# Kernel optimization log

Hardware: AMD Instinct MI355X
Metric: run time of the kernel (lower is better)

The kernel has to match this reference:

```python
import jax, jax.numpy as jnp
import numpy as np

N_NODES = 50000
N_PAIRS = 1_600_000
D_IN = 128
D_OUT = 128


def setup_inputs() -> dict:
    key = jax.random.key(0)
    k1, k2, k3, k4, k5, k6 = jax.random.split(key, 6)
    features = jax.random.normal(k1, (N_NODES, D_IN), dtype=jnp.float32)
    pair_w = jax.random.uniform(k2, (N_PAIRS,), dtype=jnp.float32)  # cosine weights per pair
    # Xavier-uniform init for the projection weight, zeros for bias (as in torch module)
    limit = float(np.sqrt(6.0 / (D_IN + D_OUT)))
    weight = jax.random.uniform(k3, (D_IN, D_OUT), dtype=jnp.float32, minval=-limit, maxval=limit)
    bias = jnp.zeros((D_OUT,), dtype=jnp.float32)
    pair_i = jax.random.randint(k4, (N_PAIRS,), 0, N_NODES)
    pair_j = jax.random.randint(k5, (N_PAIRS,), 0, N_NODES)
    node_idx = jnp.sort(jax.random.randint(k6, (N_PAIRS,), 0, N_NODES))  # center node per pair
    return {"features": features, "pair_w": pair_w, "weight": weight, "bias": bias,
            "pair_i": pair_i, "pair_j": pair_j, "node_idx": node_idx}


def reference(features, pair_w, weight, bias, pair_i, pair_j, node_idx):
    # Per pair: (features[i] + features[j]) * cos_weight  -> [n_pairs, d_in]
    msgs = (features[pair_i] + features[pair_j]) * pair_w[:, None]
    # Accumulate into the center node of each pair -> [n_nodes, d_in]
    agg = jax.ops.segment_sum(msgs, node_idx, num_segments=N_NODES)
    # Final linear projection
    return agg @ weight + bias
```

## Files before the change

### kernel.cpp

```cpp
#include <hip/hip_runtime.h>

#define D 128

__device__ __forceinline__ float bf_lo(unsigned u) { return __uint_as_float(u << 16); }
__device__ __forceinline__ float bf_hi(unsigned u) { return __uint_as_float(u & 0xffff0000u); }
__device__ __forceinline__ unsigned pack_bf16(float a, float b) {
    unsigned ua = __float_as_uint(a), ub = __float_as_uint(b);
    ua = (ua + 0x7fffu + ((ua >> 16) & 1u)) >> 16;
    ub = (ub + 0x7fffu + ((ub >> 16) & 1u)) >> 16;
    return ua | (ub << 16);
}

__global__ __launch_bounds__(256) void cvt_bf16_kernel(const float* __restrict__ F,
                                                       unsigned* __restrict__ Fb, int n4) {
    int t = blockIdx.x * 256 + threadIdx.x;
    if (t >= n4) return;
    float4 v = reinterpret_cast<const float4*>(F)[t];
    uint2 o = {pack_bf16(v.x, v.y), pack_bf16(v.z, v.w)};
    reinterpret_cast<uint2*>(Fb)[t] = o;
}

__global__ __launch_bounds__(256) void wcvt_kernel(const float* __restrict__ W,
                                                   unsigned* __restrict__ Wb) {
    int t = blockIdx.x * 256 + threadIdx.x;
    if (t >= D * D / 2) return;
    Wb[t] = pack_bf16(W[2 * t], W[2 * t + 1]);
}

__global__ void prepack_kernel(const int* __restrict__ pi, const int* __restrict__ pj,
                               const float* __restrict__ pw, const int* __restrict__ nidx,
                               uint2* __restrict__ rec, int* __restrict__ offs,
                               int n_pairs, int n_nodes) {
    int p = blockIdx.x * 256 + threadIdx.x;
    if (p >= n_pairs) return;
    rec[p] = make_uint2((unsigned)pi[p] | ((unsigned)pj[p] << 16), __float_as_uint(pw[p]));
    int cur  = nidx[p];
    int prev = p ? nidx[p - 1] : -1;
    for (int n = prev + 1; n <= cur; ++n) offs[n] = p;
    if (p == n_pairs - 1)
        for (int n = cur + 1; n <= n_nodes; ++n) offs[n] = n_pairs;
}

__global__ __launch_bounds__(256) void aggregate_kernel(
    const unsigned* __restrict__ Fb, const uint2* __restrict__ rec,
    const int* __restrict__ offs, unsigned* __restrict__ aggb, int n_nodes) {
    const int cg  = blockIdx.x & 1;
    const int wid = threadIdx.x >> 6;
    const int n   = (blockIdx.x >> 1) * 4 + wid;
    if (n >= n_nodes) return;
    const int start = offs[n];
    const int end   = offs[n + 1];
    const int lane  = threadIdx.x & 7;
    const int g     = (threadIdx.x >> 3) & 7;

    const unsigned* __restrict__ base = Fb + cg * 32 + lane * 4;

    float a0 = 0.f, a1 = 0.f, a2 = 0.f, a3 = 0.f;
    float a4 = 0.f, a5 = 0.f, a6 = 0.f, a7 = 0.f;
    for (int p = start + g; p < end; p += 8) {
        const uint2 r = rec[p];
        const unsigned i = r.x & 0xffffu;
        const unsigned j = r.x >> 16;
        const float  w = __uint_as_float(r.y);
        const uint4 ui = *reinterpret_cast<const uint4*>(base + (size_t)i * 64);
        const uint4 uj = *reinterpret_cast<const uint4*>(base + (size_t)j * 64);
        a0 += (bf_lo(ui.x) + bf_lo(uj.x)) * w;
        a1 += (bf_hi(ui.x) + bf_hi(uj.x)) * w;
        a2 += (bf_lo(ui.y) + bf_lo(uj.y)) * w;
        a3 += (bf_hi(ui.y) + bf_hi(uj.y)) * w;
        a4 += (bf_lo(ui.z) + bf_lo(uj.z)) * w;
        a5 += (bf_hi(ui.z) + bf_hi(uj.z)) * w;
        a6 += (bf_lo(ui.w) + bf_lo(uj.w)) * w;
        a7 += (bf_hi(ui.w) + bf_hi(uj.w)) * w;
    }

#pragma unroll
    for (int m = 8; m <= 32; m <<= 1) {
        a0 += __shfl_xor(a0, m); a1 += __shfl_xor(a1, m);
        a2 += __shfl_xor(a2, m); a3 += __shfl_xor(a3, m);
        a4 += __shfl_xor(a4, m); a5 += __shfl_xor(a5, m);
        a6 += __shfl_xor(a6, m); a7 += __shfl_xor(a7, m);
    }

    if (g == 0) {
        uint4 o = {pack_bf16(a0, a1), pack_bf16(a2, a3),
                   pack_bf16(a4, a5), pack_bf16(a6, a7)};
        *reinterpret_cast<uint4*>(aggb + (size_t)n * 64 + cg * 32 + lane * 4) = o;
    }
}

__global__ __launch_bounds__(256) void proj_kernel(
    const unsigned* __restrict__ aggb, const unsigned* __restrict__ Wb,
    const float* __restrict__ bias, float* __restrict__ out, int M) {
    __shared__ float    Al[64 * D];
    __shared__ unsigned Wl[D * (D / 2)];
    const int tid = threadIdx.x;

    for (int t = tid; t < D * (D / 2) / 4; t += 256)
        reinterpret_cast<uint4*>(Wl)[t] = reinterpret_cast<const uint4*>(Wb)[t];

    const int row0 = blockIdx.x * 64;
    for (int t = tid; t < 64 * 16; t += 256) {
        const int r = t >> 4, q = t & 15;
        uint4 v = {0u, 0u, 0u, 0u};
        if (row0 + r < M)
            v = reinterpret_cast<const uint4*>(aggb)[(size_t)(row0 + r) * 16 + q];
        float* dst = &Al[r * D + q * 8];
        dst[0] = bf_lo(v.x); dst[1] = bf_hi(v.x);
        dst[2] = bf_lo(v.y); dst[3] = bf_hi(v.y);
        dst[4] = bf_lo(v.z); dst[5] = bf_hi(v.z);
        dst[6] = bf_lo(v.w); dst[7] = bf_hi(v.w);
    }
    __syncthreads();

    const int tcol = tid & 31;
    const int trow = tid >> 5;
    float acc[8][4];
#pragma unroll
    for (int r = 0; r < 8; ++r)
#pragma unroll
        for (int c = 0; c < 4; ++c) acc[r][c] = 0.f;

    for (int d = 0; d < D; ++d) {
        const uint2 wu = *reinterpret_cast<const uint2*>(&Wl[d * (D / 2) + tcol * 2]);
        const float w0 = bf_lo(wu.x), w1 = bf_hi(wu.x);
        const float w2 = bf_lo(wu.y), w3 = bf_hi(wu.y);
#pragma unroll
        for (int r = 0; r < 8; ++r) {
            const float a = Al[(trow * 8 + r) * D + d];
            acc[r][0] += a * w0;
            acc[r][1] += a * w1;
            acc[r][2] += a * w2;
            acc[r][3] += a * w3;
        }
    }

    const float4 bv = *reinterpret_cast<const float4*>(&bias[tcol * 4]);
#pragma unroll
    for (int r = 0; r < 8; ++r) {
        const int row = row0 + trow * 8 + r;
        if (row < M) {
            float4 o;
            o.x = acc[r][0] + bv.x;
            o.y = acc[r][1] + bv.y;
            o.z = acc[r][2] + bv.z;
            o.w = acc[r][3] + bv.w;
            *reinterpret_cast<float4*>(&out[(size_t)row * D + tcol * 4]) = o;
        }
    }
}

extern "C" void kernel_launch(void* const* d_in, const int* in_sizes, int n_in,
                              void* d_out, int out_size, void* d_ws, size_t ws_size,
                              hipStream_t stream) {
    const float* F    = (const float*)d_in[0];
    const float* pw   = (const float*)d_in[1];
    const float* W    = (const float*)d_in[2];
    const float* bias = (const float*)d_in[3];
    const int*   pi   = (const int*)d_in[4];
    const int*   pj   = (const int*)d_in[5];
    const int*   nidx = (const int*)d_in[6];
    float* out = (float*)d_out;

    const int n_pairs = in_sizes[1];
    const int n_nodes = in_sizes[0] / D;

    const size_t aggb_bytes = (size_t)n_nodes * D * 2;
    const size_t offs_bytes = ((size_t)(n_nodes + 1) * 4 + 255) & ~(size_t)255;
    const size_t rec_bytes  = (size_t)n_pairs * 8;
    const size_t wb_bytes   = (size_t)D * (D / 2) * 4;
    const size_t fb_bytes   = (size_t)n_nodes * D * 2;

    unsigned* aggb = (unsigned*)d_ws;
    int*      offs = (int*)((char*)d_ws + aggb_bytes);
    uint2*    rec  = (uint2*)((char*)d_ws + aggb_bytes + offs_bytes);
    unsigned* Wb   = (unsigned*)((char*)d_ws + aggb_bytes + offs_bytes + rec_bytes);
    size_t used = aggb_bytes + offs_bytes + rec_bytes + wb_bytes;
    unsigned* Fb = (ws_size >= used + fb_bytes)
                 ? (unsigned*)((char*)d_ws + used)
                 : (unsigned*)d_out;

    const int n4 = n_nodes * D / 4;
    cvt_bf16_kernel<<<(n4 + 255) / 256, 256, 0, stream>>>(F, Fb, n4);
    wcvt_kernel<<<(D * D / 2 + 255) / 256, 256, 0, stream>>>(W, Wb);
    prepack_kernel<<<(n_pairs + 255) / 256, 256, 0, stream>>>(pi, pj, pw, nidx, rec, offs,
                                                              n_pairs, n_nodes);
    const int nb = (n_nodes + 3) / 4;
    aggregate_kernel<<<nb * 2, 256, 0, stream>>>(Fb, rec, offs, aggb, n_nodes);
    proj_kernel<<<(n_nodes + 63) / 64, 256, 0, stream>>>(aggb, Wb, bias, out, n_nodes);
}
```

Before: 123.1 us.

## Fuse prep kernels, shuffle-broadcast pair records, and use MFMA for projection

Merges the three preprocessing kernels into one launch with block-range dispatch and splits pair records into separate index and weight arrays. The aggregate kernel now loads 64 pair records per wave with coalesced nontemporal loads and broadcasts them via shuffles. The projection is rewritten to use bf16 MFMA 16x16x32 instructions reading operands straight from global memory, using a transposed weight layout. This cuts launch overhead and the cost of the scalar FP32 GEMM, at the price of extra shuffles and uncached operand loads.

```diff
diff --git a/kernel.cpp b/kernel.cpp
--- a/kernel.cpp
+++ b/kernel.cpp
@@ -1,6 +1,9 @@
 #include <hip/hip_runtime.h>
 
 #define D 128
+
+typedef __attribute__((ext_vector_type(8))) short short8;
+typedef __attribute__((ext_vector_type(4))) float floatx4;
 
 __device__ __forceinline__ float bf_lo(unsigned u) { return __uint_as_float(u << 16); }
 __device__ __forceinline__ float bf_hi(unsigned u) { return __uint_as_float(u & 0xffff0000u); }
@@ -11,39 +14,44 @@
     return ua | (ub << 16);
 }
 
-__global__ __launch_bounds__(256) void cvt_bf16_kernel(const float* __restrict__ F,
-                                                       unsigned* __restrict__ Fb, int n4) {
-    int t = blockIdx.x * 256 + threadIdx.x;
-    if (t >= n4) return;
-    float4 v = reinterpret_cast<const float4*>(F)[t];
-    uint2 o = {pack_bf16(v.x, v.y), pack_bf16(v.z, v.w)};
-    reinterpret_cast<uint2*>(Fb)[t] = o;
-}
-
-__global__ __launch_bounds__(256) void wcvt_kernel(const float* __restrict__ W,
-                                                   unsigned* __restrict__ Wb) {
-    int t = blockIdx.x * 256 + threadIdx.x;
-    if (t >= D * D / 2) return;
-    Wb[t] = pack_bf16(W[2 * t], W[2 * t + 1]);
-}
-
-__global__ void prepack_kernel(const int* __restrict__ pi, const int* __restrict__ pj,
-                               const float* __restrict__ pw, const int* __restrict__ nidx,
-                               uint2* __restrict__ rec, int* __restrict__ offs,
-                               int n_pairs, int n_nodes) {
-    int p = blockIdx.x * 256 + threadIdx.x;
-    if (p >= n_pairs) return;
-    rec[p] = make_uint2((unsigned)pi[p] | ((unsigned)pj[p] << 16), __float_as_uint(pw[p]));
-    int cur  = nidx[p];
-    int prev = p ? nidx[p - 1] : -1;
-    for (int n = prev + 1; n <= cur; ++n) offs[n] = p;
-    if (p == n_pairs - 1)
-        for (int n = cur + 1; n <= n_nodes; ++n) offs[n] = n_pairs;
+__global__ __launch_bounds__(256) void prep_kernel(
+    const float* __restrict__ F, const float* __restrict__ pw,
+    const float* __restrict__ W, const int* __restrict__ pi,
+    const int* __restrict__ pj, const int* __restrict__ nidx,
+    unsigned* __restrict__ Fb, unsigned* __restrict__ ij,
+    float* __restrict__ wv, int* __restrict__ offs, unsigned* __restrict__ Wt,
+    int n_nodes, int n_pairs) {
+    const int B1 = (n_nodes * (D / 4) + 255) / 256;
+    const int B2 = (n_pairs + 255) / 256;
+    const int b = blockIdx.x;
+    if (b < B1) {
+        int t = b * 256 + threadIdx.x;
+        if (t >= n_nodes * (D / 4)) return;
+        float4 v = reinterpret_cast<const float4*>(F)[t];
+        uint2 o = {pack_bf16(v.x, v.y), pack_bf16(v.z, v.w)};
+        reinterpret_cast<uint2*>(Fb)[t] = o;
+    } else if (b < B1 + B2) {
+        int p = (b - B1) * 256 + threadIdx.x;
+        if (p >= n_pairs) return;
+        ij[p] = (unsigned)pi[p] | ((unsigned)pj[p] << 16);
+        wv[p] = pw[p];
+        int cur  = nidx[p];
+        int prev = p ? nidx[p - 1] : -1;
+        for (int n = prev + 1; n <= cur; ++n) offs[n] = p;
+        if (p == n_pairs - 1)
+            for (int n = cur + 1; n <= n_nodes; ++n) offs[n] = n_pairs;
+    } else {
+        int t = (b - B1 - B2) * 256 + threadIdx.x;
+        if (t >= D * (D / 2)) return;
+        int c = t >> 6, kk = t & 63;
+        Wt[t] = pack_bf16(W[(2 * kk) * D + c], W[(2 * kk + 1) * D + c]);
+    }
 }
 
 __global__ __launch_bounds__(256) void aggregate_kernel(
-    const unsigned* __restrict__ Fb, const uint2* __restrict__ rec,
-    const int* __restrict__ offs, unsigned* __restrict__ aggb, int n_nodes) {
+    const unsigned* __restrict__ Fb, const unsigned* __restrict__ ij,
+    const float* __restrict__ wv, const int* __restrict__ offs,
+    unsigned* __restrict__ aggb, int n_nodes) {
     const int cg  = blockIdx.x & 1;
     const int wid = threadIdx.x >> 6;
     const int n   = (blockIdx.x >> 1) * 4 + wid;
@@ -52,26 +60,42 @@
     const int end   = offs[n + 1];
     const int lane  = threadIdx.x & 7;
     const int g     = (threadIdx.x >> 3) & 7;
+    const int l64   = threadIdx.x & 63;
 
     const unsigned* __restrict__ base = Fb + cg * 32 + lane * 4;
 
     float a0 = 0.f, a1 = 0.f, a2 = 0.f, a3 = 0.f;
     float a4 = 0.f, a5 = 0.f, a6 = 0.f, a7 = 0.f;
-    for (int p = start + g; p < end; p += 8) {
-        const uint2 r = rec[p];
-        const unsigned i = r.x & 0xffffu;
-        const unsigned j = r.x >> 16;
-        const float  w = __uint_as_float(r.y);
-        const uint4 ui = *reinterpret_cast<const uint4*>(base + (size_t)i * 64);
-        const uint4 uj = *reinterpret_cast<const uint4*>(base + (size_t)j * 64);
-        a0 += (bf_lo(ui.x) + bf_lo(uj.x)) * w;
-        a1 += (bf_hi(ui.x) + bf_hi(uj.x)) * w;
-        a2 += (bf_lo(ui.y) + bf_lo(uj.y)) * w;
-        a3 += (bf_hi(ui.y) + bf_hi(uj.y)) * w;
-        a4 += (bf_lo(ui.z) + bf_lo(uj.z)) * w;
-        a5 += (bf_hi(ui.z) + bf_hi(uj.z)) * w;
-        a6 += (bf_lo(ui.w) + bf_lo(uj.w)) * w;
-        a7 += (bf_hi(ui.w) + bf_hi(uj.w)) * w;
+
+    for (int c0 = start; c0 < end; c0 += 64) {
+        const int myp = c0 + l64;
+        unsigned ijv = 0u;
+        float    wvv = 0.f;
+        if (myp < end) {
+            ijv = __builtin_nontemporal_load(ij + myp);
+            wvv = __builtin_nontemporal_load(wv + myp);
+        }
+        const int nsteps = min(8, (end - c0 + 7) >> 3);
+        for (int s = 0; s < nsteps; ++s) {
+            const int src = s * 8 + g;
+            const unsigned r = __shfl(ijv, src);
+            const float    w = __shfl(wvv, src);
+            const int p = c0 + src;
+            if (p < end) {
+                const unsigned i = r & 0xffffu;
+                const unsigned j = r >> 16;
+                const uint4 ui = *reinterpret_cast<const uint4*>(base + (size_t)i * 64);
+                const uint4 uj = *reinterpret_cast<const uint4*>(base + (size_t)j * 64);
+                a0 += (bf_lo(ui.x) + bf_lo(uj.x)) * w;
+                a1 += (bf_hi(ui.x) + bf_hi(uj.x)) * w;
+                a2 += (bf_lo(ui.y) + bf_lo(uj.y)) * w;
+                a3 += (bf_hi(ui.y) + bf_hi(uj.y)) * w;
+                a4 += (bf_lo(ui.z) + bf_lo(uj.z)) * w;
+                a5 += (bf_hi(ui.z) + bf_hi(uj.z)) * w;
+                a6 += (bf_lo(ui.w) + bf_lo(uj.w)) * w;
+                a7 += (bf_hi(ui.w) + bf_hi(uj.w)) * w;
+            }
+        }
     }
 
 #pragma unroll
@@ -90,62 +114,42 @@
 }
 
 __global__ __launch_bounds__(256) void proj_kernel(
-    const unsigned* __restrict__ aggb, const unsigned* __restrict__ Wb,
+    const unsigned* __restrict__ aggb, const unsigned* __restrict__ Wt,
     const float* __restrict__ bias, float* __restrict__ out, int M) {
-    __shared__ float    Al[64 * D];
-    __shared__ unsigned Wl[D * (D / 2)];
-    const int tid = threadIdx.x;
+    const int wid = threadIdx.x >> 6;
+    const int l   = threadIdx.x & 63;
+    const int lr  = l & 15;
+    const int lk  = l >> 4;
+    const int row_base = blockIdx.x * 64 + wid * 16;
 
-    for (int t = tid; t < D * (D / 2) / 4; t += 256)
-        reinterpret_cast<uint4*>(Wl)[t] = reinterpret_cast<const uint4*>(Wb)[t];
+    int arow = row_base + lr;
+    if (arow >= M) arow = M - 1;
 
-    const int row0 = blockIdx.x * 64;
-    for (int t = tid; t < 64 * 16; t += 256) {
-        const int r = t >> 4, q = t & 15;
-        uint4 v = {0u, 0u, 0u, 0u};
-        if (row0 + r < M)
-            v = reinterpret_cast<const uint4*>(aggb)[(size_t)(row0 + r) * 16 + q];
-        float* dst = &Al[r * D + q * 8];
-        dst[0] = bf_lo(v.x); dst[1] = bf_hi(v.x);
-        dst[2] = bf_lo(v.y); dst[3] = bf_hi(v.y);
-        dst[4] = bf_lo(v.z); dst[5] = bf_hi(v.z);
-        dst[6] = bf_lo(v.w); dst[7] = bf_hi(v.w);
-    }
-    __syncthreads();
+    const short8* __restrict__ A8 = reinterpret_cast<const short8*>(aggb);
+    const short8* __restrict__ B8 = reinterpret_cast<const short8*>(Wt);
 
-    const int tcol = tid & 31;
-    const int trow = tid >> 5;
-    float acc[8][4];
+    floatx4 acc[8];
 #pragma unroll
-    for (int r = 0; r < 8; ++r)
+    for (int t = 0; t < 8; ++t) acc[t] = (floatx4){0.f, 0.f, 0.f, 0.f};
+
 #pragma unroll
-        for (int c = 0; c < 4; ++c) acc[r][c] = 0.f;
-
-    for (int d = 0; d < D; ++d) {
-        const uint2 wu = *reinterpret_cast<const uint2*>(&Wl[d * (D / 2) + tcol * 2]);
-        const float w0 = bf_lo(wu.x), w1 = bf_hi(wu.x);
-        const float w2 = bf_lo(wu.y), w3 = bf_hi(wu.y);
+    for (int ks = 0; ks < 4; ++ks) {
+        const short8 a = A8[(size_t)arow * 16 + ks * 4 + lk];
 #pragma unroll
-        for (int r = 0; r < 8; ++r) {
-            const float a = Al[(trow * 8 + r) * D + d];
-            acc[r][0] += a * w0;
-            acc[r][1] += a * w1;
-            acc[r][2] += a * w2;
-            acc[r][3] += a * w3;
+        for (int t = 0; t < 8; ++t) {
+            const short8 bfr = B8[(size_t)(t * 16 + lr) * 16 + ks * 4 + lk];
+            acc[t] = __builtin_amdgcn_mfma_f32_16x16x32_bf16(a, bfr, acc[t], 0, 0, 0);
         }
     }
 
-    const float4 bv = *reinterpret_cast<const float4*>(&bias[tcol * 4]);
 #pragma unroll
-    for (int r = 0; r < 8; ++r) {
-        const int row = row0 + trow * 8 + r;
-        if (row < M) {
-            float4 o;
-            o.x = acc[r][0] + bv.x;
-            o.y = acc[r][1] + bv.y;
-            o.z = acc[r][2] + bv.z;
-            o.w = acc[r][3] + bv.w;
-            *reinterpret_cast<float4*>(&out[(size_t)row * D + tcol * 4]) = o;
+    for (int t = 0; t < 8; ++t) {
+        const float bcol = bias[t * 16 + lr];
+#pragma unroll
+        for (int r = 0; r < 4; ++r) {
+            const int row = row_base + lk * 4 + r;
+            if (row < M)
+                out[(size_t)row * D + t * 16 + lr] = acc[t][r] + bcol;
         }
     }
 }
@@ -167,25 +171,29 @@
 
     const size_t aggb_bytes = (size_t)n_nodes * D * 2;
     const size_t offs_bytes = ((size_t)(n_nodes + 1) * 4 + 255) & ~(size_t)255;
-    const size_t rec_bytes  = (size_t)n_pairs * 8;
-    const size_t wb_bytes   = (size_t)D * (D / 2) * 4;
+    const size_t ij_bytes   = (size_t)n_pairs * 4;
+    const size_t wv_bytes   = (size_t)n_pairs * 4;
+    const size_t wt_bytes   = (size_t)D * (D / 2) * 4;
     const size_t fb_bytes   = (size_t)n_nodes * D * 2;
 
-    unsigned* aggb = (unsigned*)d_ws;
-    int*      offs = (int*)((char*)d_ws + aggb_bytes);
-    uint2*    rec  = (uint2*)((char*)d_ws + aggb_bytes + offs_bytes);
-    unsigned* Wb   = (unsigned*)((char*)d_ws + aggb_bytes + offs_bytes + rec_bytes);
-    size_t used = aggb_bytes + offs_bytes + rec_bytes + wb_bytes;
+    char* p = (char*)d_ws;
+    unsigned* aggb = (unsigned*)p;                 p += aggb_bytes;
+    int*      offs = (int*)p;                      p += offs_bytes;
+    unsigned* ij   = (unsigned*)p;                 p += ij_bytes;
+    float*    wvv  = (float*)p;                    p += wv_bytes;
+    unsigned* Wt   = (unsigned*)p;                 p += wt_bytes;
+    size_t used = (size_t)(p - (char*)d_ws);
     unsigned* Fb = (ws_size >= used + fb_bytes)
-                 ? (unsigned*)((char*)d_ws + used)
+                 ? (unsigned*)p
                  : (unsigned*)d_out;
 
-    const int n4 = n_nodes * D / 4;
-    cvt_bf16_kernel<<<(n4 + 255) / 256, 256, 0, stream>>>(F, Fb, n4);
-    wcvt_kernel<<<(D * D / 2 + 255) / 256, 256, 0, stream>>>(W, Wb);
-    prepack_kernel<<<(n_pairs + 255) / 256, 256, 0, stream>>>(pi, pj, pw, nidx, rec, offs,
-                                                              n_pairs, n_nodes);
+    const int B1 = (n_nodes * (D / 4) + 255) / 256;
+    const int B2 = (n_pairs + 255) / 256;
+    const int B3 = (D * (D / 2) + 255) / 256;
+    prep_kernel<<<B1 + B2 + B3, 256, 0, stream>>>(F, pw, W, pi, pj, nidx,
+                                                  Fb, ij, wvv, offs, Wt,
+                                                  n_nodes, n_pairs);
     const int nb = (n_nodes + 3) / 4;
-    aggregate_kernel<<<nb * 2, 256, 0, stream>>>(Fb, rec, offs, aggb, n_nodes);
-    proj_kernel<<<(n_nodes + 63) / 64, 256, 0, stream>>>(aggb, Wb, bias, out, n_nodes);
+    aggregate_kernel<<<nb * 2, 256, 0, stream>>>(Fb, ij, wvv, offs, aggb, n_nodes);
+    proj_kernel<<<(n_nodes + 63) / 64, 256, 0, stream>>>(aggb, Wt, bias, out, n_nodes);
 }
```

Measured after the change: 108.8 us. 11.6% less time.
